# Optimization experiments

Hardware: AMD Instinct MI355X
Metric: run time of the kernel (lower is better)

The kernel has to match this reference:

```python
import jax, jax.numpy as jnp
import numpy as np

PATCHES = [(4, 4), (2, 2)]  # (width, height) per stream chunk
SCALE = 2
DM = 256


def conv2d(x, w, bias, pad=0):
    y = jax.lax.conv_general_dilated(
        x, w, window_strides=(1, 1), padding=[(pad, pad), (pad, pad)],
        dimension_numbers=("NCHW", "OIHW", "NCHW"))
    return y + bias[None, :, None, None]


def to_patches(x, b, t, dk, out_h, ph, out_w, pw):
    # x: [b*t, dk, out_h*ph, out_w*pw] -> [b, t*out_h*out_w, dk*ph*pw]
    x = x.reshape(b, t, dk, out_h, ph, out_w, pw)
    return x.transpose(0, 1, 3, 5, 2, 4, 6).reshape(b, t * out_h * out_w, dk * ph * pw)


def from_patches(y, b, t, dk, out_h, ph, out_w, pw):
    # y: [b, t*out_h*out_w, dk*ph*pw] -> [b*t, dk, out_h*ph, out_w*pw]
    y = y.reshape(b, t, out_h, out_w, dk, ph, pw)
    return y.transpose(0, 1, 4, 2, 5, 3, 6).reshape(b * t, dk, out_h * ph, out_w * pw)


def attention(q, k, v):
    d = q.shape[-1]
    scores = jnp.einsum("bnd,bmd->bnm", q, k) / jnp.sqrt(jnp.asarray(d, q.dtype))
    p = jax.nn.softmax(scores, axis=-1)
    return jnp.einsum("bnm,bmd->bnd", p, v)


def forward(x_lo, x_hi, b,
            wq_lo, bq_lo, wk_lo, bk_lo, wv_lo, bv_lo,
            wq_hi, bq_hi, wk_hi, bk_hi, wv_hi, bv_hi,
            wo_lo, bo_lo, wo_hi, bo_hi):
    bt_lo, _, h, w = x_lo.shape
    bt_hi, _, h_, w_ = x_hi.shape
    t_lo = bt_lo // b
    t_hi = bt_hi // b
    n_p = len(PATCHES)
    d_k_lo = DM * SCALE ** 2 // n_p
    d_k_hi = DM // n_p

    q_lo_all = conv2d(x_lo, wq_lo, bq_lo)
    k_lo_all = conv2d(x_lo, wk_lo, bk_lo)
    v_lo_all = conv2d(x_lo, wv_lo, bv_lo)
    q_hi_all = conv2d(x_hi, wq_hi, bq_hi)
    k_hi_all = conv2d(x_hi, wk_hi, bk_hi)
    v_hi_all = conv2d(x_hi, wv_hi, bv_hi)

    outs_lo, outs_hi = [], []
    for i, (width, height) in enumerate(PATCHES):
        out_w, out_h = w // width, h // height
        sl_lo = slice(i * d_k_lo, (i + 1) * d_k_lo)
        sl_hi = slice(i * d_k_hi, (i + 1) * d_k_hi)
        ql = to_patches(q_lo_all[:, sl_lo], b, t_lo, d_k_lo, out_h, height, out_w, width)
        kl = to_patches(k_lo_all[:, sl_lo], b, t_lo, d_k_lo, out_h, height, out_w, width)
        vl = to_patches(v_lo_all[:, sl_lo], b, t_lo, d_k_lo, out_h, height, out_w, width)
        qh = to_patches(q_hi_all[:, sl_hi], b, t_hi, d_k_hi, out_h, height * SCALE, out_w, width * SCALE)
        kh = to_patches(k_hi_all[:, sl_hi], b, t_hi, d_k_hi, out_h, height * SCALE, out_w, width * SCALE)
        vh = to_patches(v_hi_all[:, sl_hi], b, t_hi, d_k_hi, out_h, height * SCALE, out_w, width * SCALE)

        q = jnp.concatenate([ql, qh], axis=1)
        k = jnp.concatenate([kl, kh], axis=1)
        v = jnp.concatenate([vl, vh], axis=1)
        y = attention(q, k, v)

        n_lo = t_lo * out_h * out_w
        y_lo = from_patches(y[:, :n_lo], b, t_lo, d_k_lo, out_h, height, out_w, width)
        y_hi = from_patches(y[:, n_lo:], b, t_hi, d_k_hi, out_h, height * SCALE, out_w, width * SCALE)
        outs_lo.append(y_lo)
        outs_hi.append(y_hi)

    out_lo = jnp.concatenate(outs_lo, axis=1)
    out_hi = jnp.concatenate(outs_hi, axis=1)
    out_lo = jax.nn.leaky_relu(conv2d(out_lo, wo_lo, bo_lo, pad=1), 0.2)
    out_hi = jax.nn.leaky_relu(conv2d(out_hi, wo_hi, bo_hi, pad=1), 0.2)
    return out_lo, out_hi


def setup_inputs() -> dict:
    key = jax.random.key(0)
    ks = jax.random.split(key, 12)
    dm2 = DM * SCALE ** 2  # 1024
    s = 0.02
    inp = {
        "x_lo": jax.random.normal(ks[0], (16, DM, 32, 32), jnp.float32),
        "x_hi": jax.random.normal(ks[1], (16, DM, 64, 64), jnp.float32),
        "b": 4,
        "wq_lo": jax.random.normal(ks[2], (dm2, DM, 1, 1), jnp.float32) * s,
        "bq_lo": jnp.zeros((dm2,), jnp.float32),
        "wk_lo": jax.random.normal(ks[3], (dm2, DM, 1, 1), jnp.float32) * s,
        "bk_lo": jnp.zeros((dm2,), jnp.float32),
        "wv_lo": jax.random.normal(ks[4], (dm2, DM, 1, 1), jnp.float32) * s,
        "bv_lo": jnp.zeros((dm2,), jnp.float32),
        "wq_hi": jax.random.normal(ks[5], (DM, DM, 1, 1), jnp.float32) * s,
        "bq_hi": jnp.zeros((DM,), jnp.float32),
        "wk_hi": jax.random.normal(ks[6], (DM, DM, 1, 1), jnp.float32) * s,
        "bk_hi": jnp.zeros((DM,), jnp.float32),
        "wv_hi": jax.random.normal(ks[7], (DM, DM, 1, 1), jnp.float32) * s,
        "bv_hi": jnp.zeros((DM,), jnp.float32),
        "wo_lo": jax.random.normal(ks[8], (DM, dm2, 3, 3), jnp.float32) * s,
        "bo_lo": jnp.zeros((DM,), jnp.float32),
        "wo_hi": jax.random.normal(ks[9], (DM, DM, 3, 3), jnp.float32) * s,
        "bo_hi": jnp.zeros((DM,), jnp.float32),
    }
    return inp


def reference(x_lo, x_hi, b,
              wq_lo, bq_lo, wk_lo, bk_lo, wv_lo, bv_lo,
              wq_hi, bq_hi, wk_hi, bk_hi, wv_hi, bv_hi,
              wo_lo, bo_lo, wo_hi, bo_hi):
    return forward(x_lo, x_hi, b,
                   wq_lo, bq_lo, wk_lo, bk_lo, wv_lo, bv_lo,
                   wq_hi, bq_hi, wk_hi, bk_hi, wv_hi, bv_hi,
                   wo_lo, bo_lo, wo_hi, bo_hi)
```

## Files before the change

### kernel.cpp

```cpp
#include <hip/hip_runtime.h>
#include <hip/hip_bf16.h>
#include <stdint.h>

typedef __attribute__((ext_vector_type(8))) short short8;
typedef __attribute__((ext_vector_type(4))) short short4v;
typedef __attribute__((ext_vector_type(2))) short short2v;
typedef __attribute__((ext_vector_type(4))) float floatx4;

__device__ __forceinline__ unsigned short f2b(float f) {
  unsigned u = __builtin_bit_cast(unsigned, f);
  unsigned r = u + 0x7fffu + ((u >> 16) & 1u);
  return (unsigned short)(r >> 16);
}
__device__ __forceinline__ float b2f(unsigned short h) {
  unsigned u = ((unsigned)h) << 16;
  return __builtin_bit_cast(float, u);
}
__device__ __forceinline__ void glds16(const unsigned short* src, unsigned short* dst) {
  __builtin_amdgcn_global_load_lds((const __attribute__((address_space(1))) void*)src,
                                   (__attribute__((address_space(3))) void*)dst, 16, 0, 0);
}
__device__ __forceinline__ int swz(int r, int o) {
  return (r << 9) + (o ^ ((((o >> 7) & 3) ^ (r & 7)) << 4));
}
__device__ __forceinline__ void xcd_remap(int& bx, int& by, int& bz) {
  const int gx = gridDim.x, gy = gridDim.y;
  const int nwg = gx * gy * (int)gridDim.z;
  int lin = bx + gx * (by + gy * bz);
  lin = (lin & 7) * (nwg >> 3) + (lin >> 3);
  bx = lin % gx; const int r = lin / gx;
  by = r % gy; bz = r / gy;
}

struct GemmP {
  const unsigned short* A;
  const unsigned short* B;
  long sAb, sBb;
  int lda, ldb, K;
  unsigned short* C; long sCb; int ldc;
  const float* bias;
  unsigned short *Q0, *K0, *V0t, *Q1, *K1, *V1t;
};

template<int EPI>
__global__ __launch_bounds__(512) void gemm256(GemmP p) {
  __shared__ __align__(16) unsigned short LDS[65536];
  const int tid = threadIdx.x;
  const int wv = tid >> 6, lane = tid & 63;
  const int wm = wv >> 2, wn = wv & 3;
  const int g = lane >> 4, l16 = lane & 15;
  int bx = blockIdx.x, by = blockIdx.y, bz = blockIdx.z;
  xcd_remap(bx, by, bz);
  const int m0 = by * 256, n0 = bx * 256;

  int bb = bz, koff = 0, Keff = p.K;
  if constexpr (EPI == 1) { bb = bz >> 4; koff = (bz & 15) * (p.K >> 4); Keff = p.K >> 4; }
  const unsigned short* Ab = p.A + (long)bb * p.sAb + (long)m0 * p.lda + koff;
  const unsigned short* Bb = p.B + (long)bb * p.sBb + (long)n0 * p.ldb + koff;
  const int NT = Keff >> 5;

  const int r0 = tid >> 2;
  const int cs = (tid & 3) ^ ((r0 >> 1) & 3);
  const unsigned short* aS0 = Ab + (long)r0 * p.lda + cs * 8;
  const unsigned short* aS1 = aS0 + (long)128 * p.lda;
  const unsigned short* bS0 = Bb + (long)r0 * p.ldb + cs * 8;
  const unsigned short* bS1 = bS0 + (long)128 * p.ldb;
  unsigned short* const lds0 = (unsigned short*)LDS;
  const int wbase = wv * 512;

  auto STAGE_A = [&](int t) {
    unsigned short* d = lds0 + (t & 3) * 16384;
    const long ko = (long)t * 32;
    glds16(aS0 + ko, d + wbase);
    glds16(aS1 + ko, d + 4096 + wbase);
  };
  auto STAGE_B = [&](int t) {
    unsigned short* d = lds0 + (t & 3) * 16384 + 8192;
    const long ko = (long)t * 32;
    glds16(bS0 + ko, d + wbase);
    glds16(bS1 + ko, d + 4096 + wbase);
  };

  STAGE_A(0); STAGE_B(0); STAGE_A(1); STAGE_B(1); STAGE_A(2); STAGE_B(2);

  floatx4 acc[8][4];
  const floatx4 z4 = {0.f, 0.f, 0.f, 0.f};
#pragma unroll
  for (int i = 0; i < 8; ++i)
#pragma unroll
    for (int j = 0; j < 4; ++j) acc[i][j] = z4;

  const int loff = l16 * 32 + ((g ^ ((l16 >> 1) & 3)) * 8);
  const int aRowB = wm * 128;

  for (int t = 0; t < NT; ++t) {
    const unsigned short* As = lds0 + (t & 3) * 16384;
    const unsigned short* Bs = As + 8192;
    if (t < NT - 2)        asm volatile("s_waitcnt vmcnt(8)" ::: "memory");
    else if (t == NT - 2)  asm volatile("s_waitcnt vmcnt(4)" ::: "memory");
    else                   asm volatile("s_waitcnt vmcnt(0)" ::: "memory");
    __builtin_amdgcn_s_barrier();
    __builtin_amdgcn_sched_barrier(0);
    if (t + 3 < NT) STAGE_A(t + 3);
    short8 bf[4], af[4], ag[4];
#pragma unroll
    for (int ni = 0; ni < 4; ++ni)
      bf[ni] = *(const short8*)(Bs + (wn * 64 + ni * 16) * 32 + loff);
#pragma unroll
    for (int mi = 0; mi < 4; ++mi)
      af[mi] = *(const short8*)(As + (aRowB + mi * 16) * 32 + loff);
#pragma unroll
    for (int mi = 0; mi < 4; ++mi)
      ag[mi] = *(const short8*)(As + (aRowB + 64 + mi * 16) * 32 + loff);
    __builtin_amdgcn_s_setprio(1);
#pragma unroll
    for (int mi = 0; mi < 4; ++mi)
#pragma unroll
      for (int ni = 0; ni < 4; ++ni)
        acc[mi][ni] = __builtin_amdgcn_mfma_f32_16x16x32_bf16(af[mi], bf[ni], acc[mi][ni], 0, 0, 0);
    __builtin_amdgcn_s_setprio(0);
    if (t + 3 < NT) STAGE_B(t + 3);
    __builtin_amdgcn_s_setprio(1);
#pragma unroll
    for (int mi = 0; mi < 4; ++mi)
#pragma unroll
      for (int ni = 0; ni < 4; ++ni)
        acc[4 + mi][ni] = __builtin_amdgcn_mfma_f32_16x16x32_bf16(ag[mi], bf[ni], acc[4 + mi][ni], 0, 0, 0);
    __builtin_amdgcn_s_setprio(0);
  }

  if constexpr (EPI == 1) {
    unsigned short* C = p.C + (long)bz * p.sCb;
#pragma unroll
    for (int mi = 0; mi < 8; ++mi) {
#pragma unroll
      for (int ni = 0; ni < 4; ++ni) {
        const int col = n0 + wn * 64 + ni * 16 + l16;
#pragma unroll
        for (int r4 = 0; r4 < 4; ++r4) {
          const int row = m0 + wm * 128 + mi * 16 + g * 4 + r4;
          C[(long)row * p.ldc + col] = f2b(acc[mi][ni][r4]);
        }
      }
    }
  } else {
    __syncthreads();
    char* shb = (char*)LDS;
    const int sel = (EPI == 2) ? (m0 >> 10) : (m0 >> 8);
#pragma unroll
    for (int mi = 0; mi < 8; ++mi) {
#pragma unroll
      for (int ni = 0; ni < 4; ++ni) {
        const int c = wn * 64 + ni * 16 + l16;
#pragma unroll
        for (int r4 = 0; r4 < 4; ++r4) {
          const int rr = wm * 128 + mi * 16 + g * 4 + r4;
          float v = acc[mi][ni][r4];
          if constexpr (EPI == 2 || EPI == 3) {
            v += p.bias[m0 + rr];
            if (sel == 0) {
              float sc;
              if constexpr (EPI == 2) sc = ((m0 & 1023) < 512) ? 0.011048543456039806f
                                                               : 0.02209708691207961f;
              else                    sc = (rr < 128) ? 0.011048543456039806f
                                                      : 0.02209708691207961f;
              v *= sc;
            }
          }
          *(unsigned short*)(shb + swz(rr, c * 2)) = f2b(v);
        }
      }
    }
    __syncthreads();

    if constexpr (EPI == 0) {
      unsigned short* C = p.C + (long)bz * p.sCb;
#pragma unroll
      for (int j = 0; j < 16; ++j) {
        const int e = j * 512 + tid;
        const int r = e >> 5, ck = e & 31;
        short8 v = *(const short8*)(shb + swz(r, ck * 16));
        *(short8*)(C + (long)(m0 + r) * p.ldc + n0 + ck * 8) = v;
      }
    } else if constexpr (EPI == 2) {
      const int chb = m0 & 1023;
      const bool cfg0 = chb < 512;
      const int b = bz >> 2, tt = bz & 3;
      const int k0 = n0 >> 8;
      unsigned short* dst = cfg0 ? (sel == 0 ? p.Q0 : sel == 1 ? p.K0 : p.V0t)
                                 : (sel == 0 ? p.Q1 : sel == 1 ? p.K1 : p.V1t);
      if (sel != 2) {
        if (cfg0) {
          const long base = (long)(b * 512) * 8192;
#pragma unroll
          for (int j = 0; j < 16; ++j) {
            const int e = j * 512 + tid;
            const int pi = e >> 9, idx2 = e & 511;
            const int ch = idx2 >> 1, hf = idx2 & 1;
            const int oyL = pi >> 3, ox = pi & 7;
            const int nseq = (tt * 8 + 2 * k0 + oyL) * 8 + ox;
            const int yl = oyL * 4 + hf * 2;
            short4v a = *(const short4v*)(shb + swz(ch, (yl * 32 + ox * 4) * 2));
            short4v b2 = *(const short4v*)(shb + swz(ch, ((yl + 1) * 32 + ox * 4) * 2));
            short8 v = {a[0], a[1], a[2], a[3], b2[0], b2[1], b2[2], b2[3]};
            *(short8*)(dst + base + (long)nseq * 8192 + (chb + ch) * 16 + hf * 8) = v;
          }
        } else {
          const int c2lo = chb - 512;
          const long base = (long)(b * 2048) * 2048;
#pragma unroll
          for (int j = 0; j < 16; ++j) {
            const int e = j * 512 + tid;
            const int pi = e >> 7, cp = e & 127;
            const int oyL = pi >> 4, ox = pi & 15;
            const int nseq = (tt * 16 + 4 * k0 + oyL) * 16 + ox;
            short8 v;
#pragma unroll
            for (int rr = 0; rr < 2; ++rr) {
#pragma unroll
              for (int k = 0; k < 2; ++k) {
                short2v pr = *(const short2v*)(shb +
                    swz(cp * 2 + rr, ((oyL * 2 + k) * 32 + ox * 2) * 2));
                v[rr * 4 + k * 2] = pr[0];
                v[rr * 4 + k * 2 + 1] = pr[1];
              }
            }
            *(short8*)(dst + base + (long)nseq * 2048 + (c2lo + cp * 2) * 4) = v;
          }
        }
      } else {
        if (cfg0) {
          const long base = (long)(b * 8192) * 512;
#pragma unroll
          for (int j = 0; j < 16; ++j) {
            const int e = j * 512 + tid;
            const int oyL = e >> 12, fu = e & 4095;
            const int ch = fu >> 4, pp = fu & 15;
            const int py = pp >> 2, px = pp & 3;
            const int yl = oyL * 4 + py;
            short8 v;
#pragma unroll
            for (int ox = 0; ox < 8; ++ox)
              v[ox] = *(const unsigned short*)(shb + swz(ch, (yl * 32 + ox * 4 + px) * 2));
            const long f = (long)(chb + ch) * 16 + pp;
            *(short8*)(dst + base + f * 512 + (tt * 8 + 2 * k0 + oyL) * 8) = v;
          }
        } else {
          const int c2lo = chb - 512;
          const long base = (long)(b * 2048) * 2048;
#pragma unroll
          for (int j = 0; j < 16; ++j) {
            const int e = j * 512 + tid;
            const int he = e & 1, oyL = (e >> 1) & 3, fu = e >> 3;
            const int c2 = fu >> 2, pp = fu & 3;
            const int py = pp >> 1, px = pp & 1;
            const int yl = oyL * 2 + py;
            short8 v;
#pragma unroll
            for (int i = 0; i < 8; ++i) {
              const int ox = he * 8 + i;
              v[i] = *(const unsigned short*)(shb + swz(c2, (yl * 32 + ox * 2 + px) * 2));
            }
            const long f = (long)(c2lo + c2) * 4 + pp;
            *(short8*)(dst + base + f * 2048 + (tt * 16 + 4 * k0 + oyL) * 16 + he * 8) = v;
          }
        }
      }
    } else if constexpr (EPI == 3) {
      const int b = bz >> 2, tt = bz & 3;
      const int k0 = n0 >> 8;
      const int oyA = k0 >> 1, pyb = (k0 & 1) * 4;
      unsigned short* dstA = sel == 0 ? p.Q0 : sel == 1 ? p.K0 : p.V0t;
      unsigned short* dstB = sel == 0 ? p.Q1 : sel == 1 ? p.K1 : p.V1t;
      if (sel != 2) {
#pragma unroll
        for (int j = 0; j < 16; ++j) {
          const int e = j * 512 + tid;
          if (e < 4096) {
            const int ox = e >> 9, cy = e & 511;
            const int ch = cy >> 2, yl = cy & 3;
            const int nseq = 256 + (tt * 8 + oyA) * 8 + ox;
            short8 v = *(const short8*)(shb + swz(ch, (yl * 64 + ox * 8) * 2));
            *(short8*)(dstA + ((long)(b * 512 + nseq)) * 8192 + ch * 64 + (pyb + yl) * 8) = v;
          } else {
            const int ee = e - 4096;
            const int ox = ee >> 8, cc = ee & 255;
            const int c2 = cc >> 1, hf = cc & 1;
            const int nseq = 1024 + (tt * 16 + k0) * 16 + ox;
            short8 v;
#pragma unroll
            for (int k = 0; k < 2; ++k) {
              short4v a = *(const short4v*)(shb +
                  swz(128 + c2, ((hf * 2 + k) * 64 + ox * 4) * 2));
              v[k * 4] = a[0]; v[k * 4 + 1] = a[1]; v[k * 4 + 2] = a[2]; v[k * 4 + 3] = a[3];
            }
            *(short8*)(dstB + ((long)(b * 2048 + nseq)) * 2048 + c2 * 16 + hf * 8) = v;
          }
        }
      } else {
#pragma unroll
        for (int j = 0; j < 16; ++j) {
          const int e = j * 512 + tid;
          if (e < 4096) {
            const int ch = e >> 5, yl = (e >> 3) & 3, px = e & 7;
            short8 v;
#pragma unroll
            for (int ox = 0; ox < 8; ++ox)
              v[ox] = *(const unsigned short*)(shb + swz(ch, (yl * 64 + ox * 8 + px) * 2));
            const long f = (long)ch * 64 + (pyb + yl) * 8 + px;
            *(short8*)(dstA + ((long)b * 8192 + f) * 512 + 256 + (tt * 8 + oyA) * 8) = v;
          } else {
            const int ee = e - 4096;
            const int he = ee & 1, fu = ee >> 1;
            const int c2 = fu >> 4, pp = fu & 15;
            const int py = pp >> 2, px = pp & 3;
            short8 v;
#pragma unroll
            for (int i = 0; i < 8; ++i) {
              const int x = (he * 8 + i) * 4 + px;
              v[i] = *(const unsigned short*)(shb + swz(128 + c2, (py * 64 + x) * 2));
            }
            const long f = (long)c2 * 16 + pp;
            *(short8*)(dstB + ((long)b * 2048 + f) * 2048 + 1024 + (tt * 16 + k0) * 16 + he * 8) = v;
          }
        }
      }
    }
  }
}

template<int H, int W, int CIN, int KS, bool PARTIAL>
__global__ __launch_bounds__(512) void conv256(const unsigned short* __restrict__ Cinp,
                                               const unsigned short* __restrict__ Wt,
                                               const float* __restrict__ bias,
                                               float* __restrict__ out,
                                               unsigned short* __restrict__ P0,
                                               unsigned short* __restrict__ P1) {
  constexpr int HP = H + 2, WP = W + 2;
  constexpr int CC = CIN / KS;
  constexpr int NT = 9 * CC / 32;
  __shared__ __align__(16) unsigned short LDS[65536];
  const int tid = threadIdx.x;
  const int wv = tid >> 6, lane = tid & 63;
  const int wm = wv >> 2, wn = wv & 3;
  const int g = lane >> 4, l16 = lane & 15;
  int bx = blockIdx.x, by = blockIdx.y, bz = blockIdx.z;
  xcd_remap(bx, by, bz);
  const int bt = bz / KS, ks = bz % KS;
  const int n0 = bx * 256;

  const int r0 = tid >> 2;
  const int cs = (tid & 3) ^ ((r0 >> 1) & 3);
  const unsigned short* wA0 = Wt + (long)r0 * CIN + ks * CC + cs * 8;
  const unsigned short* wA1 = wA0 + (long)128 * CIN;
  const int p0 = n0 + r0, p1 = p0 + 128;
  const int y0p = p0 / W, x0p = p0 % W;
  const int y1p = p1 / W, x1p = p1 % W;
  const unsigned short* cB = Cinp + (long)bt * HP * WP * CIN + ks * CC + cs * 8;
  const unsigned short* pB0 = cB + ((long)y0p * WP + x0p) * CIN;
  const unsigned short* pB1 = cB + ((long)y1p * WP + x1p) * CIN;
  unsigned short* const lds0 = (unsigned short*)LDS;
  const int wbase = wv * 512;

  auto STAGE_A = [&](int t) {
    unsigned short* d = lds0 + (t & 3) * 16384;
    const int tap = t >> 3, tc = (t & 7) * 32;
    const long off = (long)tap * (256L * CIN) + tc;
    glds16(wA0 + off, d + wbase);
    glds16(wA1 + off, d + 4096 + wbase);
  };
  auto STAGE_B = [&](int t) {
    unsigned short* d = lds0 + (t & 3) * 16384 + 8192;
    const int tap = t >> 3, tc = (t & 7) * 32;
    const int ky = tap / 3, kx = tap - ky * 3;
    const long off = ((long)ky * WP + kx) * CIN + tc;
    glds16(pB0 + off, d + wbase);
    glds16(pB1 + off, d + 4096 + wbase);
  };

  STAGE_A(0); STAGE_B(0); STAGE_A(1); STAGE_B(1); STAGE_A(2); STAGE_B(2);

  floatx4 acc[8][4];
  const floatx4 z4 = {0.f, 0.f, 0.f, 0.f};
#pragma unroll
  for (int i = 0; i < 8; ++i)
#pragma unroll
    for (int j = 0; j < 4; ++j) acc[i][j] = z4;

  const int loff = l16 * 32 + ((g ^ ((l16 >> 1) & 3)) * 8);
  const int aRowB = wm * 128;

  for (int t = 0; t < NT; ++t) {
    const unsigned short* As = lds0 + (t & 3) * 16384;
    const unsigned short* Bs = As + 8192;
    if (t < NT - 2)        asm volatile("s_waitcnt vmcnt(8)" ::: "memory");
    else if (t == NT - 2)  asm volatile("s_waitcnt vmcnt(4)" ::: "memory");
    else                   asm volatile("s_waitcnt vmcnt(0)" ::: "memory");
    __builtin_amdgcn_s_barrier();
    __builtin_amdgcn_sched_barrier(0);
    if (t + 3 < NT) STAGE_A(t + 3);
    short8 bf[4], af[4], ag[4];
#pragma unroll
    for (int ni = 0; ni < 4; ++ni)
      bf[ni] = *(const short8*)(Bs + (wn * 64 + ni * 16) * 32 + loff);
#pragma unroll
    for (int mi = 0; mi < 4; ++mi)
      af[mi] = *(const short8*)(As + (aRowB + mi * 16) * 32 + loff);
#pragma unroll
    for (int mi = 0; mi < 4; ++mi)
      ag[mi] = *(const short8*)(As + (aRowB + 64 + mi * 16) * 32 + loff);
    __builtin_amdgcn_s_setprio(1);
#pragma unroll
    for (int mi = 0; mi < 4; ++mi)
#pragma unroll
      for (int ni = 0; ni < 4; ++ni)
        acc[mi][ni] = __builtin_amdgcn_mfma_f32_16x16x32_bf16(af[mi], bf[ni], acc[mi][ni], 0, 0, 0);
    __builtin_amdgcn_s_setprio(0);
    if (t + 3 < NT) STAGE_B(t + 3);
    __builtin_amdgcn_s_setprio(1);
#pragma unroll
    for (int mi = 0; mi < 4; ++mi)
#pragma unroll
      for (int ni = 0; ni < 4; ++ni)
        acc[4 + mi][ni] = __builtin_amdgcn_mfma_f32_16x16x32_bf16(ag[mi], bf[ni], acc[4 + mi][ni], 0, 0, 0);
    __builtin_amdgcn_s_setprio(0);
  }

  if constexpr (!PARTIAL) {
#pragma unroll
    for (int mi = 0; mi < 8; ++mi) {
#pragma unroll
      for (int ni = 0; ni < 4; ++ni) {
        const int pn = n0 + wn * 64 + ni * 16 + l16;
        const int y = pn / W, x = pn % W;
#pragma unroll
        for (int r4 = 0; r4 < 4; ++r4) {
          const int co = wm * 128 + mi * 16 + g * 4 + r4;
          float v = acc[mi][ni][r4] + bias[co];
          v = v > 0.f ? v : 0.2f * v;
          out[(((long)bt * 256 + co) * H + y) * W + x] = v;
        }
      }
    }
  } else {
    unsigned short* pout = (ks < 2 ? P0 : P1) + (long)(ks & 1) * (16L * 256 * H * W);
#pragma unroll
    for (int mi = 0; mi < 8; ++mi) {
#pragma unroll
      for (int ni = 0; ni < 4; ++ni) {
        const int pn = n0 + wn * 64 + ni * 16 + l16;
        const int y = pn / W, x = pn % W;
#pragma unroll
        for (int r4 = 0; r4 < 4; ++r4) {
          const int co = wm * 128 + mi * 16 + g * 4 + r4;
          pout[(((long)bt * 256 + co) * H + y) * W + x] = f2b(acc[mi][ni][r4]);
        }
      }
    }
  }
}

template<int L>
__global__ __launch_bounds__(256) void softmax_rows(unsigned short* S) {
  const int w = threadIdx.x >> 6, lane = threadIdx.x & 63;
  const long row = (long)blockIdx.x * 4 + w;
  unsigned short* R = S + row * L;
  constexpr int NC = L / 64;
  float v[NC];
  float m = -1e30f;
#pragma unroll
  for (int i = 0; i < NC; ++i) { v[i] = b2f(R[i * 64 + lane]); m = fmaxf(m, v[i]); }
#pragma unroll
  for (int off = 32; off; off >>= 1) m = fmaxf(m, __shfl_xor(m, off, 64));
  float s = 0.f;
#pragma unroll
  for (int i = 0; i < NC; ++i) { v[i] = __expf(v[i] - m); s += v[i]; }
#pragma unroll
  for (int off = 32; off; off >>= 1) s += __shfl_xor(s, off, 64);
  const float inv = 1.0f / s;
#pragma unroll
  for (int i = 0; i < NC; ++i) R[i * 64 + lane] = f2b(v[i] * inv);
}

__global__ __launch_bounds__(256) void softmax_red16(const unsigned short* __restrict__ P,
                                                     unsigned short* __restrict__ S) {
  const int w = threadIdx.x >> 6, lane = threadIdx.x & 63;
  const int rowg = blockIdx.x * 4 + w;
  const int b = rowg >> 9, n = rowg & 511;
  const unsigned short* base = P + ((long)b * 16) * 262144 + (long)n * 512 + lane;
  float v[8];
#pragma unroll
  for (int i = 0; i < 8; ++i) {
    float s = 0.f;
#pragma unroll
    for (int ks = 0; ks < 16; ++ks) s += b2f(base[(long)ks * 262144 + i * 64]);
    v[i] = s;
  }
  float m = -1e30f;
#pragma unroll
  for (int i = 0; i < 8; ++i) m = fmaxf(m, v[i]);
#pragma unroll
  for (int off = 32; off; off >>= 1) m = fmaxf(m, __shfl_xor(m, off, 64));
  float s = 0.f;
#pragma unroll
  for (int i = 0; i < 8; ++i) { v[i] = __expf(v[i] - m); s += v[i]; }
#pragma unroll
  for (int off = 32; off; off >>= 1) s += __shfl_xor(s, off, 64);
  const float inv = 1.0f / s;
  unsigned short* R = S + (long)rowg * 512;
#pragma unroll
  for (int i = 0; i < 8; ++i) R[i * 64 + lane] = f2b(v[i] * inv);
}

__global__ __launch_bounds__(256) void xt_kernel(const float* __restrict__ x,
                                                 unsigned short* __restrict__ xt, int NPIX) {
  __shared__ unsigned short tile[64 * 65];
  const int tid = threadIdx.x;
  const int bt = blockIdx.z, ch0 = blockIdx.y * 64;
  const long pix0 = (long)blockIdx.x * 64;
  const float* src = x + ((long)bt * 256 + ch0) * NPIX + pix0;
#pragma unroll
  for (int i = 0; i < 16; ++i) {
    const int lin = i * 256 + tid;
    const int ch = lin >> 6, px = lin & 63;
    tile[ch * 65 + px] = f2b(src[(long)ch * NPIX + px]);
  }
  __syncthreads();
  unsigned short* dst = xt + ((long)bt * NPIX + pix0) * 256 + ch0;
#pragma unroll
  for (int i = 0; i < 16; ++i) {
    const int lin = i * 256 + tid;
    const int px = lin >> 6, ch = lin & 63;
    dst[(long)px * 256 + ch] = tile[ch * 65 + px];
  }
}

__global__ void prep_qkv_w(const float* wq, const float* wk, const float* wv,
                           const float* bq, const float* bk, const float* bv,
                           unsigned short* Wcat, float* Bcat, int CO) {
  const int idx = blockIdx.x * 256 + threadIdx.x;
  const int n = 3 * CO * 256;
  if (idx < n) {
    const int sel = idx / (CO * 256);
    const int r = idx - sel * CO * 256;
    const float* wsel = sel == 0 ? wq : (sel == 1 ? wk : wv);
    Wcat[idx] = f2b(wsel[r]);
  }
  if (idx < 3 * CO) {
    const int sel = idx / CO;
    const int r = idx - sel * CO;
    const float* bsel = sel == 0 ? bq : (sel == 1 ? bk : bv);
    Bcat[idx] = bsel[r];
  }
}

__global__ void prep_conv_w(const float* wo, unsigned short* Wt, int CIN) {
  const int idx = blockIdx.x * 256 + threadIdx.x;
  const int n = 9 * 256 * CIN;
  if (idx < n) {
    const int t9 = idx / (256 * CIN);
    const int rem = idx - t9 * 256 * CIN;
    const int o = rem / CIN, i = rem - o * CIN;
    Wt[idx] = f2b(wo[((long)o * CIN + i) * 9 + t9]);
  }
}

__global__ __launch_bounds__(256) void zero_border(unsigned short* buf, int HP, int WP, int C) {
  const long i = (long)blockIdx.x * 256 + threadIdx.x;
  const int per_px = C >> 3;
  const int strip = 2 * WP + 2 * (HP - 2);
  const long tot = (long)16 * strip * per_px;
  if (i >= tot) return;
  const int c8 = (int)(i % per_px);
  const long r = i / per_px;
  const int s = (int)(r % strip);
  const int bt = (int)(r / strip);
  int y, x;
  if (s < WP) { y = 0; x = s; }
  else if (s < 2 * WP) { y = HP - 1; x = s - WP; }
  else if (s < 2 * WP + (HP - 2)) { y = s - 2 * WP + 1; x = 0; }
  else { y = s - 2 * WP - (HP - 2) + 1; x = WP - 1; }
  const short8 z = {0, 0, 0, 0, 0, 0, 0, 0};
  *(short8*)(buf + (((long)bt * HP + y) * WP + x) * C + c8 * 8) = z;
}

__global__ __launch_bounds__(256) void repackY0(const unsigned short* __restrict__ Y0,
                                                unsigned short* __restrict__ CinLo,
                                                unsigned short* __restrict__ CinHi) {
  __shared__ __align__(16) unsigned short T[8704];
  const int r = blockIdx.x;
  const int b = r >> 9, n = r & 511;
  const int tid = threadIdx.x;
  const int wv2 = tid >> 6, lane = tid & 63;
  const unsigned short* row = Y0 + (long)r * 8192;
  if (n < 256) {
#pragma unroll
    for (int q = 0; q < 4; ++q) {
      short8 v = *(const short8*)(row + tid * 32 + q * 8);
#pragma unroll
      for (int j = 0; j < 8; ++j) {
        const int f = tid * 32 + q * 8 + j;
        T[(f & 15) * 520 + (f >> 4)] = (unsigned short)v[j];
      }
    }
    __syncthreads();
    const int t = n >> 6, oh = (n >> 3) & 7, ow = n & 7;
    const int bt = b * 4 + t;
#pragma unroll
    for (int it = 0; it < 4; ++it) {
      const int pp = it * 4 + wv2;
      const int py = pp >> 2, px = pp & 3;
      short8 v = *(const short8*)(T + pp * 520 + lane * 8);
      *(short8*)(CinLo + (((long)bt * 34 + oh * 4 + py + 1) * 34 + ow * 4 + px + 1) * 1024
                 + lane * 8) = v;
    }
  } else {
    const int m = n - 256;
#pragma unroll
    for (int q = 0; q < 4; ++q) {
      short8 v = *(const short8*)(row + tid * 32 + q * 8);
#pragma unroll
      for (int j = 0; j < 8; ++j) {
        const int f = tid * 32 + q * 8 + j;
        T[(f & 63) * 136 + (f >> 6)] = (unsigned short)v[j];
      }
    }
    __syncthreads();
    const int t = m >> 6, oh = (m >> 3) & 7, ow = m & 7;
    const int bt = b * 4 + t;
#pragma unroll
    for (int it = 0; it < 4; ++it) {
      const int pp = it * 16 + wv2 * 4 + (lane >> 4);
      const int py = pp >> 3, px = pp & 7;
      short8 v = *(const short8*)(T + pp * 136 + (lane & 15) * 8);
      *(short8*)(CinHi + (((long)bt * 66 + oh * 8 + py + 1) * 66 + ow * 8 + px + 1) * 256
                 + (lane & 15) * 8) = v;
    }
  }
}

__global__ __launch_bounds__(256) void repackY1(const unsigned short* __restrict__ Y1,
                                                unsigned short* __restrict__ CinLo,
                                                unsigned short* __restrict__ CinHi) {
  __shared__ __align__(16) unsigned short T[2176];
  const int r = blockIdx.x;
  const int b = r >> 11, n = r & 2047;
  const int tid = threadIdx.x;
  const int wv2 = tid >> 6, lane = tid & 63;
  const unsigned short* row = Y1 + (long)r * 2048;
  short8 v = *(const short8*)(row + tid * 8);
  if (n < 1024) {
#pragma unroll
    for (int j = 0; j < 8; ++j) {
      const int f = tid * 8 + j;
      T[(f & 3) * 520 + (f >> 2)] = (unsigned short)v[j];
    }
    __syncthreads();
    const int t = n >> 8, oh = (n >> 4) & 15, ow = n & 15;
    const int bt = b * 4 + t;
    const int pp = wv2, py = pp >> 1, px = pp & 1;
    short8 o = *(const short8*)(T + pp * 520 + lane * 8);
    *(short8*)(CinLo + (((long)bt * 34 + oh * 2 + py + 1) * 34 + ow * 2 + px + 1) * 1024
               + 512 + lane * 8) = o;
  } else {
    const int m = n - 1024;
#pragma unroll
    for (int j = 0; j < 8; ++j) {
      const int f = tid * 8 + j;
      T[(f & 15) * 136 + (f >> 4)] = (unsigned short)v[j];
    }
    __syncthreads();
    const int t = m >> 8, oh = (m >> 4) & 15, ow = m & 15;
    const int bt = b * 4 + t;
    const int pp = wv2 * 4 + (lane >> 4), py = pp >> 2, px = pp & 3;
    short8 o = *(const short8*)(T + pp * 136 + (lane & 15) * 8);
    *(short8*)(CinHi + (((long)bt * 66 + oh * 4 + py + 1) * 66 + ow * 4 + px + 1) * 256
               + 128 + (lane & 15) * 8) = o;
  }
}

__global__ __launch_bounds__(256) void reduce_lrelu(const unsigned short* __restrict__ P0,
                                                    const unsigned short* __restrict__ P1,
                                                    const float* __restrict__ bias,
                                                    float* __restrict__ out) {
  const long i = (long)blockIdx.x * 256 + threadIdx.x;
  const long flat = i * 8;
  constexpr long SL = 4194304;
  short8 a = *(const short8*)(P0 + flat);
  short8 b = *(const short8*)(P0 + SL + flat);
  short8 c = *(const short8*)(P1 + flat);
  short8 d = *(const short8*)(P1 + SL + flat);
  const int co = ((int)(flat >> 10)) & 255;
  const float bv = bias[co];
  floatx4 r0, r1;
#pragma unroll
  for (int j = 0; j < 8; ++j) {
    float v = b2f((unsigned short)a[j]) + b2f((unsigned short)b[j]) +
              b2f((unsigned short)c[j]) + b2f((unsigned short)d[j]) + bv;
    v = v > 0.f ? v : 0.2f * v;
    if (j < 4) r0[j] = v; else r1[j - 4] = v;
  }
  *(floatx4*)(out + flat) = r0;
  *(floatx4*)(out + flat + 4) = r1;
}

extern "C" void kernel_launch(void* const* d_in, const int* in_sizes, int n_in,
                              void* d_out, int out_size, void* d_ws, size_t ws_size,
                              hipStream_t stream) {
  (void)in_sizes; (void)n_in; (void)out_size; (void)ws_size;
  const float* x_lo = (const float*)d_in[0];
  const float* x_hi = (const float*)d_in[1];
  const float* wq_lo = (const float*)d_in[3];
  const float* bq_lo = (const float*)d_in[4];
  const float* wk_lo = (const float*)d_in[5];
  const float* bk_lo = (const float*)d_in[6];
  const float* wv_lo = (const float*)d_in[7];
  const float* bv_lo = (const float*)d_in[8];
  const float* wq_hi = (const float*)d_in[9];
  const float* bq_hi = (const float*)d_in[10];
  const float* wk_hi = (const float*)d_in[11];
  const float* bk_hi = (const float*)d_in[12];
  const float* wv_hi = (const float*)d_in[13];
  const float* bv_hi = (const float*)d_in[14];
  const float* wo_lo = (const float*)d_in[15];
  const float* bo_lo = (const float*)d_in[16];
  const float* wo_hi = (const float*)d_in[17];
  const float* bo_hi = (const float*)d_in[18];
  float* out = (float*)d_out;

  char* ws = (char*)d_ws;
  const long B0 = 33554432;
  unsigned short* Qp0 = (unsigned short*)(ws);
  unsigned short* Kp0 = (unsigned short*)(ws + B0);
  unsigned short* V0t = (unsigned short*)(ws + 2 * B0);
  unsigned short* Qp1 = (unsigned short*)(ws + 3 * B0);
  unsigned short* Kp1 = (unsigned short*)(ws + 4 * B0);
  unsigned short* V1t = (unsigned short*)(ws + 5 * B0);
  char* ptr = ws + 6 * B0;
  unsigned short* S0 = (unsigned short*)ptr;     ptr += 2097152;
  unsigned short* Xt_lo = (unsigned short*)ptr;  ptr += 8388608;
  unsigned short* Xt_hi = (unsigned short*)ptr;  ptr += 33554432;
  unsigned short* Wcat_lo = (unsigned short*)ptr; ptr += 1572864;
  unsigned short* Wcat_hi = (unsigned short*)ptr; ptr += 393216;
  float* Bcat_lo = (float*)ptr;                  ptr += 12288;
  float* Bcat_hi = (float*)ptr;                  ptr += 3072;
  unsigned short* Wt_lo = (unsigned short*)ptr;  ptr += 4718592;
  unsigned short* Wt_hi = (unsigned short*)ptr;  ptr += 1179648;
  unsigned short* S1 = Kp0;
  unsigned short* Y0 = Qp0;
  unsigned short* Y1 = Qp1;
  unsigned short* CinP_lo = Kp0;
  unsigned short* CinP_hi = Kp1;
  unsigned short* S0p = Xt_hi;
  unsigned short* PC0 = Qp0;
  unsigned short* PC1 = Qp1;

  prep_qkv_w<<<(3 * 1024 * 256 + 255) / 256, 256, 0, stream>>>(
      wq_lo, wk_lo, wv_lo, bq_lo, bk_lo, bv_lo, Wcat_lo, Bcat_lo, 1024);
  prep_qkv_w<<<(3 * 256 * 256 + 255) / 256, 256, 0, stream>>>(
      wq_hi, wk_hi, wv_hi, bq_hi, bk_hi, bv_hi, Wcat_hi, Bcat_hi, 256);
  prep_conv_w<<<(9 * 256 * 1024 + 255) / 256, 256, 0, stream>>>(wo_lo, Wt_lo, 1024);
  prep_conv_w<<<(9 * 256 * 256 + 255) / 256, 256, 0, stream>>>(wo_hi, Wt_hi, 256);
  xt_kernel<<<dim3(16, 4, 16), 256, 0, stream>>>(x_lo, Xt_lo, 1024);
  xt_kernel<<<dim3(64, 4, 16), 256, 0, stream>>>(x_hi, Xt_hi, 4096);

  {
    GemmP p{};
    p.A = Wcat_lo; p.B = Xt_lo; p.sAb = 0; p.sBb = 1024L * 256;
    p.lda = 256; p.ldb = 256; p.K = 256;
    p.bias = Bcat_lo;
    p.Q0 = Qp0; p.K0 = Kp0; p.V0t = V0t; p.Q1 = Qp1; p.K1 = Kp1; p.V1t = V1t;
    gemm256<2><<<dim3(4, 12, 16), 512, 0, stream>>>(p);
    p.A = Wcat_hi; p.B = Xt_hi; p.sBb = 4096L * 256; p.bias = Bcat_hi;
    gemm256<3><<<dim3(16, 3, 16), 512, 0, stream>>>(p);
  }

  {
    GemmP s{};
    s.A = Qp0; s.B = Kp0; s.sAb = 512L * 8192; s.sBb = 512L * 8192;
    s.lda = 8192; s.ldb = 8192; s.K = 8192;
    s.C = S0p; s.sCb = 262144; s.ldc = 512;
    gemm256<1><<<dim3(2, 2, 64), 512, 0, stream>>>(s);
    softmax_red16<<<512, 256, 0, stream>>>(S0p, S0);
    GemmP pv{};
    pv.A = S0; pv.B = V0t; pv.sAb = 512L * 512; pv.sBb = 8192L * 512;
    pv.lda = 512; pv.ldb = 512; pv.K = 512;
    pv.C = Y0; pv.sCb = 512L * 8192; pv.ldc = 8192;
    gemm256<0><<<dim3(32, 2, 4), 512, 0, stream>>>(pv);
  }

  {
    GemmP s{};
    s.A = Qp1; s.B = Kp1; s.sAb = 2048L * 2048; s.sBb = 2048L * 2048;
    s.lda = 2048; s.ldb = 2048; s.K = 2048;
    s.C = S1; s.sCb = 2048L * 2048; s.ldc = 2048;
    gemm256<0><<<dim3(8, 8, 4), 512, 0, stream>>>(s);
    softmax_rows<2048><<<2048, 256, 0, stream>>>(S1);
    GemmP pv{};
    pv.A = S1; pv.B = V1t; pv.sAb = 2048L * 2048; pv.sBb = 2048L * 2048;
    pv.lda = 2048; pv.ldb = 2048; pv.K = 2048;
    pv.C = Y1; pv.sCb = 2048L * 2048; pv.ldc = 2048;
    gemm256<0><<<dim3(8, 8, 4), 512, 0, stream>>>(pv);
  }

  zero_border<<<1056, 256, 0, stream>>>(CinP_lo, 34, 34, 1024);
  zero_border<<<520, 256, 0, stream>>>(CinP_hi, 66, 66, 256);
  repackY0<<<2048, 256, 0, stream>>>(Y0, CinP_lo, CinP_hi);
  repackY1<<<8192, 256, 0, stream>>>(Y1, CinP_lo, CinP_hi);

  conv256<32, 32, 1024, 4, true><<<dim3(4, 1, 64), 512, 0, stream>>>(
      CinP_lo, Wt_lo, bo_lo, out, PC0, PC1);
  reduce_lrelu<<<2048, 256, 0, stream>>>(PC0, PC1, bo_lo, out);
  conv256<64, 64, 256, 1, false><<<dim3(16, 1, 16), 512, 0, stream>>>(
      CinP_hi, Wt_hi, bo_hi, out + 4194304, nullptr, nullptr);
}
```

Baseline: 554.7 us.

## Prefetch next K-step LDS fragments into registers during current MFMA block

In both the GEMM and 3x3 conv kernels, the B and first-half A fragments for step t+1 are now read from LDS during the second MFMA half of step t. Before the loop, a prologue waits on the first stage and loads the initial fragments. The vmcnt wait is tightened so the next stage's data is present before those early reads. This hides LDS read latency behind MFMA work, at the cost of extra VGPR pressure and stricter global-load waits.

```diff
diff --git a/kernel.cpp b/kernel.cpp
--- a/kernel.cpp
+++ b/kernel.cpp
@@ -93,22 +93,25 @@
   const int loff = l16 * 32 + ((g ^ ((l16 >> 1) & 3)) * 8);
   const int aRowB = wm * 128;
 
+  asm volatile("s_waitcnt vmcnt(8)" ::: "memory");
+  __builtin_amdgcn_s_barrier();
+  short8 bf[4], af[4];
+#pragma unroll
+  for (int ni = 0; ni < 4; ++ni)
+    bf[ni] = *(const short8*)(lds0 + 8192 + (wn * 64 + ni * 16) * 32 + loff);
+#pragma unroll
+  for (int mi = 0; mi < 4; ++mi)
+    af[mi] = *(const short8*)(lds0 + (aRowB + mi * 16) * 32 + loff);
+
   for (int t = 0; t < NT; ++t) {
     const unsigned short* As = lds0 + (t & 3) * 16384;
-    const unsigned short* Bs = As + 8192;
-    if (t < NT - 2)        asm volatile("s_waitcnt vmcnt(8)" ::: "memory");
-    else if (t == NT - 2)  asm volatile("s_waitcnt vmcnt(4)" ::: "memory");
-    else                   asm volatile("s_waitcnt vmcnt(0)" ::: "memory");
+    const unsigned short* AsN = lds0 + ((t + 1) & 3) * 16384;
+    if (t < NT - 2) asm volatile("s_waitcnt vmcnt(4)" ::: "memory");
+    else            asm volatile("s_waitcnt vmcnt(0)" ::: "memory");
     __builtin_amdgcn_s_barrier();
     __builtin_amdgcn_sched_barrier(0);
     if (t + 3 < NT) STAGE_A(t + 3);
-    short8 bf[4], af[4], ag[4];
-#pragma unroll
-    for (int ni = 0; ni < 4; ++ni)
-      bf[ni] = *(const short8*)(Bs + (wn * 64 + ni * 16) * 32 + loff);
-#pragma unroll
-    for (int mi = 0; mi < 4; ++mi)
-      af[mi] = *(const short8*)(As + (aRowB + mi * 16) * 32 + loff);
+    short8 ag[4];
 #pragma unroll
     for (int mi = 0; mi < 4; ++mi)
       ag[mi] = *(const short8*)(As + (aRowB + 64 + mi * 16) * 32 + loff);
@@ -120,6 +123,16 @@
         acc[mi][ni] = __builtin_amdgcn_mfma_f32_16x16x32_bf16(af[mi], bf[ni], acc[mi][ni], 0, 0, 0);
     __builtin_amdgcn_s_setprio(0);
     if (t + 3 < NT) STAGE_B(t + 3);
+    short8 bfN[4], afN[4];
+    if (t + 1 < NT) {
+      const unsigned short* BsN = AsN + 8192;
+#pragma unroll
+      for (int ni = 0; ni < 4; ++ni)
+        bfN[ni] = *(const short8*)(BsN + (wn * 64 + ni * 16) * 32 + loff);
+#pragma unroll
+      for (int mi = 0; mi < 4; ++mi)
+        afN[mi] = *(const short8*)(AsN + (aRowB + mi * 16) * 32 + loff);
+    }
     __builtin_amdgcn_s_setprio(1);
 #pragma unroll
     for (int mi = 0; mi < 4; ++mi)
@@ -127,6 +140,10 @@
       for (int ni = 0; ni < 4; ++ni)
         acc[4 + mi][ni] = __builtin_amdgcn_mfma_f32_16x16x32_bf16(ag[mi], bf[ni], acc[4 + mi][ni], 0, 0, 0);
     __builtin_amdgcn_s_setprio(0);
+    if (t + 1 < NT) {
+#pragma unroll
+      for (int i = 0; i < 4; ++i) { bf[i] = bfN[i]; af[i] = afN[i]; }
+    }
   }
 
   if constexpr (EPI == 1) {
@@ -390,22 +407,25 @@
   const int loff = l16 * 32 + ((g ^ ((l16 >> 1) & 3)) * 8);
   const int aRowB = wm * 128;
 
+  asm volatile("s_waitcnt vmcnt(8)" ::: "memory");
+  __builtin_amdgcn_s_barrier();
+  short8 bf[4], af[4];
+#pragma unroll
+  for (int ni = 0; ni < 4; ++ni)
+    bf[ni] = *(const short8*)(lds0 + 8192 + (wn * 64 + ni * 16) * 32 + loff);
+#pragma unroll
+  for (int mi = 0; mi < 4; ++mi)
+    af[mi] = *(const short8*)(lds0 + (aRowB + mi * 16) * 32 + loff);
+
   for (int t = 0; t < NT; ++t) {
     const unsigned short* As = lds0 + (t & 3) * 16384;
-    const unsigned short* Bs = As + 8192;
-    if (t < NT - 2)        asm volatile("s_waitcnt vmcnt(8)" ::: "memory");
-    else if (t == NT - 2)  asm volatile("s_waitcnt vmcnt(4)" ::: "memory");
-    else                   asm volatile("s_waitcnt vmcnt(0)" ::: "memory");
+    const unsigned short* AsN = lds0 + ((t + 1) & 3) * 16384;
+    if (t < NT - 2) asm volatile("s_waitcnt vmcnt(4)" ::: "memory");
+    else            asm volatile("s_waitcnt vmcnt(0)" ::: "memory");
     __builtin_amdgcn_s_barrier();
     __builtin_amdgcn_sched_barrier(0);
     if (t + 3 < NT) STAGE_A(t + 3);
-    short8 bf[4], af[4], ag[4];
-#pragma unroll
-    for (int ni = 0; ni < 4; ++ni)
-      bf[ni] = *(const short8*)(Bs + (wn * 64 + ni * 16) * 32 + loff);
-#pragma unroll
-    for (int mi = 0; mi < 4; ++mi)
-      af[mi] = *(const short8*)(As + (aRowB + mi * 16) * 32 + loff);
+    short8 ag[4];
 #pragma unroll
     for (int mi = 0; mi < 4; ++mi)
       ag[mi] = *(const short8*)(As + (aRowB + 64 + mi * 16) * 32 + loff);
@@ -417,6 +437,16 @@
         acc[mi][ni] = __builtin_amdgcn_mfma_f32_16x16x32_bf16(af[mi], bf[ni], acc[mi][ni], 0, 0, 0);
     __builtin_amdgcn_s_setprio(0);
     if (t + 3 < NT) STAGE_B(t + 3);
+    short8 bfN[4], afN[4];
+    if (t + 1 < NT) {
+      const unsigned short* BsN = AsN + 8192;
+#pragma unroll
+      for (int ni = 0; ni < 4; ++ni)
+        bfN[ni] = *(const short8*)(BsN + (wn * 64 + ni * 16) * 32 + loff);
+#pragma unroll
+      for (int mi = 0; mi < 4; ++mi)
+        afN[mi] = *(const short8*)(AsN + (aRowB + mi * 16) * 32 + loff);
+    }
     __builtin_amdgcn_s_setprio(1);
 #pragma unroll
     for (int mi = 0; mi < 4; ++mi)
@@ -424,6 +454,10 @@
       for (int ni = 0; ni < 4; ++ni)
         acc[4 + mi][ni] = __builtin_amdgcn_mfma_f32_16x16x32_bf16(ag[mi], bf[ni], acc[4 + mi][ni], 0, 0, 0);
     __builtin_amdgcn_s_setprio(0);
+    if (t + 1 < NT) {
+#pragma unroll
+      for (int i = 0; i < 4; ++i) { bf[i] = bfN[i]; af[i] = afN[i]; }
+    }
   }
 
   if constexpr (!PARTIAL) {
```

After: 551.8 us (median of 2 runs). About the same (-0.5%).
